# Kernel tuning notes

Measured on AMD Instinct MI355X. Metric: run time of the kernel, lower is better.

## Reference

```python
import jax, jax.numpy as jnp
import numpy as np

N, M, B, C, L, H = 8192, 8192, 16, 512, 64, 8
HEAD_DIM = C // H
PER_BATCH_KEYS = M // B
MASK_VAL = -1000.0  # matches torch masked_fill_ value


def setup_inputs() -> dict:
    key0 = jax.random.key(0)
    ks = jax.random.split(key0, 8)
    query = jax.random.normal(ks[0], (N, C), jnp.float32)
    key = jax.random.normal(ks[1], (M, C), jnp.float32)
    value = jax.random.normal(ks[2], (M, C), jnp.float32)
    # xavier-ish init for projections
    in_proj_weight = jax.random.normal(ks[3], (3 * C, C), jnp.float32) * (1.0 / np.sqrt(C))
    in_proj_bias = jnp.zeros((3 * C,), jnp.float32)
    out_w = jax.random.normal(ks[4], (C, C), jnp.float32) * (1.0 / np.sqrt(C))
    out_b = jnp.zeros((C,), jnp.float32)
    index_pair = jax.random.randint(ks[5], (N, L), 0, PER_BATCH_KEYS).astype(jnp.int32)
    pad = jax.random.uniform(ks[6], (N, L)) < 0.05
    index_pair = jnp.where(pad, jnp.int32(-1), index_pair)
    query_batch_cnt = jnp.full((B,), N // B, jnp.int32)
    key_batch_cnt = jnp.full((B,), PER_BATCH_KEYS, jnp.int32)
    index_pair_batch = jnp.repeat(jnp.arange(B, dtype=jnp.int32), N // B)
    return {
        "query": query, "key": key, "value": value,
        "in_proj_weight": in_proj_weight, "in_proj_bias": in_proj_bias,
        "out_w": out_w, "out_b": out_b,
        "index_pair": index_pair, "query_batch_cnt": query_batch_cnt,
        "key_batch_cnt": key_batch_cnt, "index_pair_batch": index_pair_batch,
    }


def reference(query, key, value, in_proj_weight, in_proj_bias, out_w, out_b,
              index_pair, query_batch_cnt, key_batch_cnt, index_pair_batch):
    embed_dim = query.shape[-1]
    scaling = float(HEAD_DIM) ** -0.5
    # qkv projections (in_proj_weight is [3C, C], applied as F.linear => x @ W.T + b)
    q = (query @ in_proj_weight[:embed_dim].T + in_proj_bias[:embed_dim]) * scaling
    k = key @ in_proj_weight[embed_dim:2 * embed_dim].T + in_proj_bias[embed_dim:2 * embed_dim]
    v = value @ in_proj_weight[2 * embed_dim:].T + in_proj_bias[2 * embed_dim:]
    q = q.reshape(N, H, HEAD_DIM)
    k = k.reshape(M, H, HEAD_DIM)
    v = v.reshape(M, H, HEAD_DIM)
    # local -> global key indices: offset by start of each query's batch key block
    key_start = jnp.cumsum(key_batch_cnt) - key_batch_cnt          # (B,)
    offset = key_start[index_pair_batch]                            # (N,)
    valid = index_pair >= 0                                         # (N, L)
    gidx = jnp.where(valid, index_pair + offset[:, None], 0)        # (N, L), safe gather
    # gather-based scores: (N, L, H)
    scores = jnp.einsum("nhd,nlhd->nlh", q, k[gidx])
    scores = jnp.where(valid[..., None], scores, MASK_VAL)
    w = jax.nn.softmax(scores, axis=1)                              # softmax over neighbors L
    # weighted value sum; masked weights underflow to exactly 0 in fp32
    attn = jnp.einsum("nlh,nlhd->nhd", w, v[gidx]).reshape(N, embed_dim)
    attn = attn @ out_w.T + out_b
    return attn, w.sum(axis=-1) / H
```

## Files before the change

### kernel.cpp

```cpp
#include <hip/hip_runtime.h>
#include <hip/hip_bf16.h>
#include <math.h>

#define NQ 8192
#define MK 8192
#define CD 512
#define LN 64
#define HH 8
#define HD 64
#define BB 16

typedef short short8 __attribute__((ext_vector_type(8)));
typedef float floatx4 __attribute__((ext_vector_type(4)));

__device__ __forceinline__ unsigned short f2bf(float x) {
    unsigned int u = __builtin_bit_cast(unsigned int, x);
    return (unsigned short)((u + 0x7FFFu + ((u >> 16) & 1u)) >> 16);
}
__device__ __forceinline__ unsigned int pkbf(float lo, float hi) {
    float2 f; f.x = lo; f.y = hi;
    __hip_bfloat162 h2 = __float22bfloat162_rn(f);
    unsigned int u;
    __builtin_memcpy(&u, &h2, 4);
    return u;
}
__device__ __forceinline__ float bflo(unsigned int u) {
    return __builtin_bit_cast(float, u << 16);
}
__device__ __forceinline__ float bfhij(unsigned int u) {
    return __builtin_bit_cast(float, u);
}
__device__ __forceinline__ short8 u4s8(uint4 u) {
    short8 s; __builtin_memcpy(&s, &u, 16); return s;
}

__device__ __forceinline__ void gl_lds16(const unsigned short* g, unsigned short* l) {
    __builtin_amdgcn_global_load_lds(
        (const __attribute__((address_space(1))) unsigned int*)g,
        (__attribute__((address_space(3))) unsigned int*)l, 16, 0, 0);
}

struct ConvSeg { const float* src; unsigned short* dst; int n4; };
struct ConvArgs { ConvSeg s[5]; };

__global__ __launch_bounds__(256) void convert_bf16(ConvArgs a) {
    const int seg = blockIdx.y;
    const int i = blockIdx.x * 256 + threadIdx.x;
    if (i >= a.s[seg].n4) return;
    const float4 v = ((const float4*)a.s[seg].src)[i];
    uint2 o; o.x = pkbf(v.x, v.y); o.y = pkbf(v.z, v.w);
    ((uint2*)a.s[seg].dst)[i] = o;
}

__device__ __forceinline__ void gemm_bf_body(const unsigned short* __restrict__ A,
                                             const unsigned short* __restrict__ W,
                                             const float* __restrict__ bias,
                                             float* __restrict__ outf,
                                             unsigned short* __restrict__ outb,
                                             float scale) {
    __shared__ unsigned short As[128 * 64];
    __shared__ unsigned short Bs[128 * 64];

    const int tid  = threadIdx.x;
    const int row0 = blockIdx.x * 128;
    const int col0 = blockIdx.y * 128;

    const int w    = tid >> 6;
    const int lane = tid & 63;
    const int wr   = w >> 1;
    const int wc   = w & 1;
    const int q    = lane >> 4;
    const int ml   = lane & 15;

    const int sr = lane >> 3;
    const int sg = (lane & 7) ^ sr;
    const unsigned short* Ap = A + (size_t)(row0 + w * 32 + sr) * CD + sg * 8;
    const unsigned short* Wp = W + (size_t)(col0 + w * 32 + sr) * CD + sg * 8;
    unsigned short* Asw = &As[(w * 32) * 64];
    unsigned short* Bsw = &Bs[(w * 32) * 64];

    floatx4 acc[4][4];
#pragma unroll
    for (int i = 0; i < 4; ++i)
#pragma unroll
        for (int j = 0; j < 4; ++j)
            acc[i][j] = (floatx4){0.f, 0.f, 0.f, 0.f};

    for (int k0 = 0; k0 < CD; k0 += 64) {
        __syncthreads();
#pragma unroll
        for (int i = 0; i < 4; ++i) {
            gl_lds16(Ap + (size_t)(i * 8) * CD + k0, Asw + i * 8 * 64);
            gl_lds16(Wp + (size_t)(i * 8) * CD + k0, Bsw + i * 8 * 64);
        }
        __syncthreads();

#pragma unroll
        for (int kw = 0; kw < 2; ++kw) {
            short8 af[4], bf[4];
            const int gp = ((kw * 4 + q) ^ (ml & 7)) * 8;
#pragma unroll
            for (int mi = 0; mi < 4; ++mi)
                af[mi] = *(const short8*)&As[(wr * 64 + mi * 16 + ml) * 64 + gp];
#pragma unroll
            for (int ni = 0; ni < 4; ++ni)
                bf[ni] = *(const short8*)&Bs[(wc * 64 + ni * 16 + ml) * 64 + gp];
#pragma unroll
            for (int mi = 0; mi < 4; ++mi)
#pragma unroll
                for (int ni = 0; ni < 4; ++ni)
                    acc[mi][ni] = __builtin_amdgcn_mfma_f32_16x16x32_bf16(
                        af[mi], bf[ni], acc[mi][ni], 0, 0, 0);
        }
    }

    float bv[4];
#pragma unroll
    for (int ni = 0; ni < 4; ++ni)
        bv[ni] = bias[col0 + wc * 64 + ni * 16 + ml];
#pragma unroll
    for (int mi = 0; mi < 4; ++mi) {
#pragma unroll
        for (int ni = 0; ni < 4; ++ni) {
            const int cg = col0 + wc * 64 + ni * 16 + ml;
#pragma unroll
            for (int r = 0; r < 4; ++r) {
                const int rg = row0 + wr * 64 + mi * 16 + q * 4 + r;
                const float val = (acc[mi][ni][r] + bv[ni]) * scale;
                if (outb) outb[(size_t)rg * CD + cg] = f2bf(val);
                else      outf[(size_t)rg * CD + cg] = val;
            }
        }
    }
}

__global__ __launch_bounds__(256) void qkv_gemm(const unsigned short* __restrict__ A_bf,
                                                const unsigned short* __restrict__ w_bf,
                                                const float* __restrict__ bias,
                                                unsigned short* __restrict__ q_bf,
                                                unsigned short* __restrict__ k_bf,
                                                unsigned short* __restrict__ v_bf) {
    const int z = blockIdx.z;
    const unsigned short* A = A_bf + (size_t)z * NQ * CD;
    unsigned short* outb = (z == 0) ? q_bf : ((z == 1) ? k_bf : v_bf);
    gemm_bf_body(A, w_bf + (size_t)z * CD * CD, bias + (size_t)z * CD,
                 nullptr, outb, (z == 0) ? 0.125f : 1.0f);
}

__global__ __launch_bounds__(256) void out_gemm(const unsigned short* __restrict__ A,
                                                const unsigned short* __restrict__ W,
                                                const float* __restrict__ bias,
                                                float* __restrict__ out) {
    gemm_bf_body(A, W, bias, out, nullptr, 1.0f);
}

__global__ __launch_bounds__(512, 4) void attn_kernel(
    const unsigned short* __restrict__ q_bf,
    const unsigned short* __restrict__ k_bf,
    const unsigned short* __restrict__ v_bf,
    const int* __restrict__ index_pair,
    const int* __restrict__ key_batch_cnt,
    const int* __restrict__ index_pair_batch,
    unsigned short* __restrict__ attn_bf,
    float* __restrict__ out2) {
    const int j = blockIdx.x;
    const int n = (j & 7) * (NQ / 8) + (j >> 3);

    const int tid  = threadIdx.x;
    const int h    = tid >> 6;
    const int lane = tid & 63;
    const int quad = lane >> 4;
    const int ml   = lane & 15;

    __shared__ float wmat[HH][LN];
    __shared__ int   gs[LN];
    __shared__ unsigned long long smask;

    if (tid < LN) {
        int incl = (lane < BB) ? key_batch_cnt[lane] : 0;
#pragma unroll
        for (int d = 1; d < BB; d <<= 1) {
            const int t = __shfl_up(incl, d, 64);
            if (lane >= d) incl += t;
        }
        const int batch = index_pair_batch[n];
        int off0 = 0;
        if (batch > 0) off0 = __shfl(incl, batch - 1, 64);
        const int gi = index_pair[n * LN + lane];
        const unsigned long long vm = __ballot(gi >= 0);
        if (lane == 0) smask = vm;
        gs[lane] = (gi >= 0) ? (gi + off0) : 0;
    }
    __syncthreads();

    const char* qp = (const char*)q_bf + (size_t)n * (CD * 2) + h * (HD * 2) + quad * 16;
    const short8 bq0 = u4s8(*(const uint4*)qp);
    const short8 bq1 = u4s8(*(const uint4*)(qp + 64));

    int gr[4];
#pragma unroll
    for (int g = 0; g < 4; ++g) gr[g] = gs[g * 16 + ml];
    uint4 a0[4], a1[4];
#pragma unroll
    for (int g = 0; g < 4; ++g) {
        const char* kp = (const char*)k_bf + (size_t)gr[g] * (CD * 2) + h * (HD * 2) + quad * 16;
        a0[g] = *(const uint4*)kp;
        a1[g] = *(const uint4*)(kp + 64);
    }
    const int r  = lane >> 3;
    const int dg = lane & 7;
    uint4 vv[8];
#pragma unroll
    for (int it = 0; it < 8; ++it) {
        const unsigned int off = (unsigned int)gs[it * 8 + r] * (CD * 2)
                                 + h * (HD * 2) + dg * 16;
        vv[it] = *(const uint4*)((const char*)v_bf + off);
    }

#pragma unroll
    for (int g = 0; g < 4; ++g) {
        floatx4 sa = (floatx4){0.f, 0.f, 0.f, 0.f};
        sa = __builtin_amdgcn_mfma_f32_16x16x32_bf16(u4s8(a0[g]), bq0, sa, 0, 0, 0);
        sa = __builtin_amdgcn_mfma_f32_16x16x32_bf16(u4s8(a1[g]), bq1, sa, 0, 0, 0);
        if (ml == 0) {
#pragma unroll
            for (int rr = 0; rr < 4; ++rr) wmat[h][g * 16 + quad * 4 + rr] = sa[rr];
        }
    }

    float score = wmat[h][lane];
    if (!((smask >> lane) & 1ull)) score = -1000.0f;
    float mx = score;
#pragma unroll
    for (int o = 32; o > 0; o >>= 1) mx = fmaxf(mx, __shfl_xor(mx, o, 64));
    float e = __expf(score - mx);
    float s = e;
#pragma unroll
    for (int o = 32; o > 0; o >>= 1) s += __shfl_xor(s, o, 64);
    const float w = e / s;
    wmat[h][lane] = w;

    float a8[8] = {0.f, 0.f, 0.f, 0.f, 0.f, 0.f, 0.f, 0.f};
#pragma unroll
    for (int it = 0; it < 8; ++it) {
        const float wl = __shfl(w, it * 8 + r, 64);
        a8[0] = fmaf(wl, bflo(vv[it].x),  a8[0]);
        a8[1] = fmaf(wl, bfhij(vv[it].x), a8[1]);
        a8[2] = fmaf(wl, bflo(vv[it].y),  a8[2]);
        a8[3] = fmaf(wl, bfhij(vv[it].y), a8[3]);
        a8[4] = fmaf(wl, bflo(vv[it].z),  a8[4]);
        a8[5] = fmaf(wl, bfhij(vv[it].z), a8[5]);
        a8[6] = fmaf(wl, bflo(vv[it].w),  a8[6]);
        a8[7] = fmaf(wl, bfhij(vv[it].w), a8[7]);
    }
#pragma unroll
    for (int o = 8; o <= 32; o <<= 1)
#pragma unroll
        for (int d = 0; d < 8; ++d) a8[d] += __shfl_xor(a8[d], o, 64);
    attn_bf[(size_t)n * CD + h * HD + dg * 8 + r] = f2bf(a8[r]);

    __syncthreads();
    if (tid < LN) {
        float s8 = 0.f;
#pragma unroll
        for (int hh = 0; hh < HH; ++hh) s8 += wmat[hh][tid];
        out2[(size_t)n * LN + tid] = s8 * (1.0f / HH);
    }
}

extern "C" void kernel_launch(void* const* d_in, const int* in_sizes, int n_in,
                              void* d_out, int out_size, void* d_ws, size_t ws_size,
                              hipStream_t stream) {
    const float* query   = (const float*)d_in[0];
    const float* key     = (const float*)d_in[1];
    const float* value   = (const float*)d_in[2];
    const float* ipw     = (const float*)d_in[3];
    const float* ipb     = (const float*)d_in[4];
    const float* out_w   = (const float*)d_in[5];
    const float* out_b   = (const float*)d_in[6];
    const int*   index_pair       = (const int*)d_in[7];
    const int*   key_batch_cnt    = (const int*)d_in[9];
    const int*   index_pair_batch = (const int*)d_in[10];

    float* out = (float*)d_out;
    unsigned short* q_bf  = (unsigned short*)d_ws;
    unsigned short* k_bf  = q_bf + (size_t)NQ * CD;
    unsigned short* v_bf  = k_bf + (size_t)NQ * CD;
    unsigned short* A_bf  = v_bf + (size_t)NQ * CD;
    unsigned short* w_bf  = A_bf + (size_t)3 * NQ * CD;
    unsigned short* ow_bf = w_bf + (size_t)3 * CD * CD;
    unsigned short* attn_bf = A_bf;

    ConvArgs ca;
    ca.s[0] = {query, A_bf,                       NQ * CD / 4};
    ca.s[1] = {key,   A_bf + (size_t)NQ * CD,     NQ * CD / 4};
    ca.s[2] = {value, A_bf + (size_t)2 * NQ * CD, NQ * CD / 4};
    ca.s[3] = {ipw,   w_bf,                       3 * CD * CD / 4};
    ca.s[4] = {out_w, ow_bf,                      CD * CD / 4};
    dim3 g0(NQ * CD / 4 / 256, 5);
    convert_bf16<<<g0, 256, 0, stream>>>(ca);

    dim3 g1(NQ / 128, CD / 128, 3);
    qkv_gemm<<<g1, 256, 0, stream>>>(A_bf, w_bf, ipb, q_bf, k_bf, v_bf);

    attn_kernel<<<NQ, 512, 0, stream>>>(q_bf, k_bf, v_bf, index_pair,
                                        key_batch_cnt, index_pair_batch,
                                        attn_bf, out + (size_t)NQ * CD);

    dim3 g3(NQ / 128, CD / 128, 1);
    out_gemm<<<g3, 256, 0, stream>>>(attn_bf, ow_bf, out_b, out);
}
```

Baseline: 223.7 us.

## Assign one query per wave looping over heads; shrink GEMM tiles to 64x128

The attention kernel now processes one query per wavefront and loops over all 8 heads, so index loading, batch offset computation and the head-averaged weight sum stay in registers with no block-wide barriers. Previously one head ran per wave in a 512-thread block per query. Both GEMMs switch from 128x128 to 64x128 output tiles, doubling the block count to improve occupancy and load balance. The trade-off is less memory-level parallelism per wave in attention, since heads run sequentially, and lower data reuse per GEMM tile.

```diff
diff --git a/kernel.cpp b/kernel.cpp
--- a/kernel.cpp
+++ b/kernel.cpp
@@ -58,75 +58,74 @@
                                              float* __restrict__ outf,
                                              unsigned short* __restrict__ outb,
                                              float scale) {
-    __shared__ unsigned short As[128 * 64];
+    __shared__ unsigned short As[64 * 64];
     __shared__ unsigned short Bs[128 * 64];
 
     const int tid  = threadIdx.x;
-    const int row0 = blockIdx.x * 128;
+    const int row0 = blockIdx.x * 64;
     const int col0 = blockIdx.y * 128;
 
     const int w    = tid >> 6;
     const int lane = tid & 63;
-    const int wr   = w >> 1;
-    const int wc   = w & 1;
     const int q    = lane >> 4;
     const int ml   = lane & 15;
 
     const int sr = lane >> 3;
     const int sg = (lane & 7) ^ sr;
-    const unsigned short* Ap = A + (size_t)(row0 + w * 32 + sr) * CD + sg * 8;
+    const unsigned short* Ap = A + (size_t)(row0 + w * 16 + sr) * CD + sg * 8;
     const unsigned short* Wp = W + (size_t)(col0 + w * 32 + sr) * CD + sg * 8;
-    unsigned short* Asw = &As[(w * 32) * 64];
+    unsigned short* Asw = &As[(w * 16) * 64];
     unsigned short* Bsw = &Bs[(w * 32) * 64];
 
-    floatx4 acc[4][4];
+    floatx4 acc[4][2];
 #pragma unroll
     for (int i = 0; i < 4; ++i)
 #pragma unroll
-        for (int j = 0; j < 4; ++j)
+        for (int j = 0; j < 2; ++j)
             acc[i][j] = (floatx4){0.f, 0.f, 0.f, 0.f};
 
     for (int k0 = 0; k0 < CD; k0 += 64) {
         __syncthreads();
 #pragma unroll
-        for (int i = 0; i < 4; ++i) {
+        for (int i = 0; i < 2; ++i)
             gl_lds16(Ap + (size_t)(i * 8) * CD + k0, Asw + i * 8 * 64);
+#pragma unroll
+        for (int i = 0; i < 4; ++i)
             gl_lds16(Wp + (size_t)(i * 8) * CD + k0, Bsw + i * 8 * 64);
-        }
         __syncthreads();
 
 #pragma unroll
         for (int kw = 0; kw < 2; ++kw) {
-            short8 af[4], bf[4];
+            short8 af[4], bf[2];
             const int gp = ((kw * 4 + q) ^ (ml & 7)) * 8;
 #pragma unroll
             for (int mi = 0; mi < 4; ++mi)
-                af[mi] = *(const short8*)&As[(wr * 64 + mi * 16 + ml) * 64 + gp];
-#pragma unroll
-            for (int ni = 0; ni < 4; ++ni)
-                bf[ni] = *(const short8*)&Bs[(wc * 64 + ni * 16 + ml) * 64 + gp];
+                af[mi] = *(const short8*)&As[(mi * 16 + ml) * 64 + gp];
+#pragma unroll
+            for (int ni = 0; ni < 2; ++ni)
+                bf[ni] = *(const short8*)&Bs[(w * 32 + ni * 16 + ml) * 64 + gp];
 #pragma unroll
             for (int mi = 0; mi < 4; ++mi)
 #pragma unroll
-                for (int ni = 0; ni < 4; ++ni)
+                for (int ni = 0; ni < 2; ++ni)
                     acc[mi][ni] = __builtin_amdgcn_mfma_f32_16x16x32_bf16(
                         af[mi], bf[ni], acc[mi][ni], 0, 0, 0);
         }
     }
 
-    float bv[4];
-#pragma unroll
-    for (int ni = 0; ni < 4; ++ni)
-        bv[ni] = bias[col0 + wc * 64 + ni * 16 + ml];
+    float bv[2];
+#pragma unroll
+    for (int ni = 0; ni < 2; ++ni)
+        bv[ni] = bias[col0 + w * 32 + ni * 16 + ml];
 #pragma unroll
     for (int mi = 0; mi < 4; ++mi) {
 #pragma unroll
-        for (int ni = 0; ni < 4; ++ni) {
-            const int cg = col0 + wc * 64 + ni * 16 + ml;
-#pragma unroll
-            for (int r = 0; r < 4; ++r) {
-                const int rg = row0 + wr * 64 + mi * 16 + q * 4 + r;
-                const float val = (acc[mi][ni][r] + bv[ni]) * scale;
+        for (int ni = 0; ni < 2; ++ni) {
+            const int cg = col0 + w * 32 + ni * 16 + ml;
+#pragma unroll
+            for (int rr = 0; rr < 4; ++rr) {
+                const int rg = row0 + mi * 16 + q * 4 + rr;
+                const float val = (acc[mi][ni][rr] + bv[ni]) * scale;
                 if (outb) outb[(size_t)rg * CD + cg] = f2bf(val);
                 else      outf[(size_t)rg * CD + cg] = val;
             }
@@ -154,7 +153,7 @@
     gemm_bf_body(A, W, bias, out, nullptr, 1.0f);
 }
 
-__global__ __launch_bounds__(512, 4) void attn_kernel(
+__global__ __launch_bounds__(256) void attn_kernel(
     const unsigned short* __restrict__ q_bf,
     const unsigned short* __restrict__ k_bf,
     const unsigned short* __restrict__ v_bf,
@@ -163,109 +162,107 @@
     const int* __restrict__ index_pair_batch,
     unsigned short* __restrict__ attn_bf,
     float* __restrict__ out2) {
-    const int j = blockIdx.x;
-    const int n = (j & 7) * (NQ / 8) + (j >> 3);
-
     const int tid  = threadIdx.x;
-    const int h    = tid >> 6;
+    const int wid  = tid >> 6;
     const int lane = tid & 63;
+    const int bx   = blockIdx.x;
+    const int n    = (bx & 7) * (NQ / 8) + (bx >> 3) * 4 + wid;
+
     const int quad = lane >> 4;
     const int ml   = lane & 15;
-
-    __shared__ float wmat[HH][LN];
-    __shared__ int   gs[LN];
-    __shared__ unsigned long long smask;
-
-    if (tid < LN) {
-        int incl = (lane < BB) ? key_batch_cnt[lane] : 0;
-#pragma unroll
-        for (int d = 1; d < BB; d <<= 1) {
-            const int t = __shfl_up(incl, d, 64);
-            if (lane >= d) incl += t;
-        }
-        const int batch = index_pair_batch[n];
-        int off0 = 0;
-        if (batch > 0) off0 = __shfl(incl, batch - 1, 64);
-        const int gi = index_pair[n * LN + lane];
-        const unsigned long long vm = __ballot(gi >= 0);
-        if (lane == 0) smask = vm;
-        gs[lane] = (gi >= 0) ? (gi + off0) : 0;
+    const int r    = lane >> 3;
+    const int dg   = lane & 7;
+
+    __shared__ float sc_s[4][LN];
+    float* sc = sc_s[wid];
+
+    int cnt = (lane < BB) ? key_batch_cnt[lane] : 0;
+#pragma unroll
+    for (int d = 1; d < BB; d <<= 1) {
+        const int t = __shfl_up(cnt, d, 64);
+        if (lane >= d) cnt += t;
     }
-    __syncthreads();
-
-    const char* qp = (const char*)q_bf + (size_t)n * (CD * 2) + h * (HD * 2) + quad * 16;
-    const short8 bq0 = u4s8(*(const uint4*)qp);
-    const short8 bq1 = u4s8(*(const uint4*)(qp + 64));
-
-    int gr[4];
-#pragma unroll
-    for (int g = 0; g < 4; ++g) gr[g] = gs[g * 16 + ml];
-    uint4 a0[4], a1[4];
-#pragma unroll
-    for (int g = 0; g < 4; ++g) {
-        const char* kp = (const char*)k_bf + (size_t)gr[g] * (CD * 2) + h * (HD * 2) + quad * 16;
-        a0[g] = *(const uint4*)kp;
-        a1[g] = *(const uint4*)(kp + 64);
+    const int batch = index_pair_batch[n];
+    const int off0  = (batch > 0) ? __shfl(cnt, batch - 1, 64) : 0;
+
+    const int gi = index_pair[n * LN + lane];
+    const unsigned long long vmask = __ballot(gi >= 0);
+    const int g = (gi >= 0) ? (gi + off0) : 0;
+
+    int krow[4];
+#pragma unroll
+    for (int grp = 0; grp < 4; ++grp)
+        krow[grp] = __shfl(g, grp * 16 + ml, 64);
+    int vrow[8];
+#pragma unroll
+    for (int it = 0; it < 8; ++it)
+        vrow[it] = __shfl(g, it * 8 + r, 64);
+
+    const size_t qbase = (size_t)n * CD;
+    float s8 = 0.f;
+
+    for (int h = 0; h < HH; ++h) {
+        const char* qp = (const char*)(q_bf + qbase + h * HD) + quad * 16;
+        const uint4 bq0 = *(const uint4*)qp;
+        const uint4 bq1 = *(const uint4*)(qp + 64);
+        uint4 a0[4], a1[4];
+#pragma unroll
+        for (int grp = 0; grp < 4; ++grp) {
+            const char* kp = (const char*)(k_bf + (size_t)krow[grp] * CD + h * HD) + quad * 16;
+            a0[grp] = *(const uint4*)kp;
+            a1[grp] = *(const uint4*)(kp + 64);
+        }
+        uint4 vv[8];
+#pragma unroll
+        for (int it = 0; it < 8; ++it) {
+            const char* vp = (const char*)(v_bf + (size_t)vrow[it] * CD + h * HD) + dg * 16;
+            vv[it] = *(const uint4*)vp;
+        }
+
+#pragma unroll
+        for (int grp = 0; grp < 4; ++grp) {
+            floatx4 sa = (floatx4){0.f, 0.f, 0.f, 0.f};
+            sa = __builtin_amdgcn_mfma_f32_16x16x32_bf16(u4s8(a0[grp]), u4s8(bq0), sa, 0, 0, 0);
+            sa = __builtin_amdgcn_mfma_f32_16x16x32_bf16(u4s8(a1[grp]), u4s8(bq1), sa, 0, 0, 0);
+            if (ml == 0) {
+#pragma unroll
+                for (int rr = 0; rr < 4; ++rr) sc[grp * 16 + quad * 4 + rr] = sa[rr];
+            }
+        }
+
+        float score = sc[lane];
+        if (!((vmask >> lane) & 1ull)) score = -1000.0f;
+        float mx = score;
+#pragma unroll
+        for (int o = 32; o > 0; o >>= 1) mx = fmaxf(mx, __shfl_xor(mx, o, 64));
+        float e = __expf(score - mx);
+        float s = e;
+#pragma unroll
+        for (int o = 32; o > 0; o >>= 1) s += __shfl_xor(s, o, 64);
+        const float w = e / s;
+        s8 += w;
+
+        float a8[8] = {0.f, 0.f, 0.f, 0.f, 0.f, 0.f, 0.f, 0.f};
+#pragma unroll
+        for (int it = 0; it < 8; ++it) {
+            const float wl = __shfl(w, it * 8 + r, 64);
+            a8[0] = fmaf(wl, bflo(vv[it].x),  a8[0]);
+            a8[1] = fmaf(wl, bfhij(vv[it].x), a8[1]);
+            a8[2] = fmaf(wl, bflo(vv[it].y),  a8[2]);
+            a8[3] = fmaf(wl, bfhij(vv[it].y), a8[3]);
+            a8[4] = fmaf(wl, bflo(vv[it].z),  a8[4]);
+            a8[5] = fmaf(wl, bfhij(vv[it].z), a8[5]);
+            a8[6] = fmaf(wl, bflo(vv[it].w),  a8[6]);
+            a8[7] = fmaf(wl, bfhij(vv[it].w), a8[7]);
+        }
+#pragma unroll
+        for (int o = 8; o <= 32; o <<= 1)
+#pragma unroll
+            for (int d = 0; d < 8; ++d) a8[d] += __shfl_xor(a8[d], o, 64);
+        attn_bf[qbase + h * HD + dg * 8 + r] = f2bf(a8[r]);
     }
-    const int r  = lane >> 3;
-    const int dg = lane & 7;
-    uint4 vv[8];
-#pragma unroll
-    for (int it = 0; it < 8; ++it) {
-        const unsigned int off = (unsigned int)gs[it * 8 + r] * (CD * 2)
-                                 + h * (HD * 2) + dg * 16;
-        vv[it] = *(const uint4*)((const char*)v_bf + off);
-    }
-
-#pragma unroll
-    for (int g = 0; g < 4; ++g) {
-        floatx4 sa = (floatx4){0.f, 0.f, 0.f, 0.f};
-        sa = __builtin_amdgcn_mfma_f32_16x16x32_bf16(u4s8(a0[g]), bq0, sa, 0, 0, 0);
-        sa = __builtin_amdgcn_mfma_f32_16x16x32_bf16(u4s8(a1[g]), bq1, sa, 0, 0, 0);
-        if (ml == 0) {
-#pragma unroll
-            for (int rr = 0; rr < 4; ++rr) wmat[h][g * 16 + quad * 4 + rr] = sa[rr];
-        }
-    }
-
-    float score = wmat[h][lane];
-    if (!((smask >> lane) & 1ull)) score = -1000.0f;
-    float mx = score;
-#pragma unroll
-    for (int o = 32; o > 0; o >>= 1) mx = fmaxf(mx, __shfl_xor(mx, o, 64));
-    float e = __expf(score - mx);
-    float s = e;
-#pragma unroll
-    for (int o = 32; o > 0; o >>= 1) s += __shfl_xor(s, o, 64);
-    const float w = e / s;
-    wmat[h][lane] = w;
-
-    float a8[8] = {0.f, 0.f, 0.f, 0.f, 0.f, 0.f, 0.f, 0.f};
-#pragma unroll
-    for (int it = 0; it < 8; ++it) {
-        const float wl = __shfl(w, it * 8 + r, 64);
-        a8[0] = fmaf(wl, bflo(vv[it].x),  a8[0]);
-        a8[1] = fmaf(wl, bfhij(vv[it].x), a8[1]);
-        a8[2] = fmaf(wl, bflo(vv[it].y),  a8[2]);
-        a8[3] = fmaf(wl, bfhij(vv[it].y), a8[3]);
-        a8[4] = fmaf(wl, bflo(vv[it].z),  a8[4]);
-        a8[5] = fmaf(wl, bfhij(vv[it].z), a8[5]);
-        a8[6] = fmaf(wl, bflo(vv[it].w),  a8[6]);
-        a8[7] = fmaf(wl, bfhij(vv[it].w), a8[7]);
-    }
-#pragma unroll
-    for (int o = 8; o <= 32; o <<= 1)
-#pragma unroll
-        for (int d = 0; d < 8; ++d) a8[d] += __shfl_xor(a8[d], o, 64);
-    attn_bf[(size_t)n * CD + h * HD + dg * 8 + r] = f2bf(a8[r]);
-
-    __syncthreads();
-    if (tid < LN) {
-        float s8 = 0.f;
-#pragma unroll
-        for (int hh = 0; hh < HH; ++hh) s8 += wmat[hh][tid];
-        out2[(size_t)n * LN + tid] = s8 * (1.0f / HH);
-    }
+
+    out2[(size_t)n * LN + lane] = s8 * (1.0f / HH);
 }
 
 extern "C" void kernel_launch(void* const* d_in, const int* in_sizes, int n_in,
@@ -300,13 +297,13 @@
     dim3 g0(NQ * CD / 4 / 256, 5);
     convert_bf16<<<g0, 256, 0, stream>>>(ca);
 
-    dim3 g1(NQ / 128, CD / 128, 3);
+    dim3 g1(NQ / 64, CD / 128, 3);
     qkv_gemm<<<g1, 256, 0, stream>>>(A_bf, w_bf, ipb, q_bf, k_bf, v_bf);
 
-    attn_kernel<<<NQ, 512, 0, stream>>>(q_bf, k_bf, v_bf, index_pair,
-                                        key_batch_cnt, index_pair_batch,
-                                        attn_bf, out + (size_t)NQ * CD);
-
-    dim3 g3(NQ / 128, CD / 128, 1);
+    attn_kernel<<<NQ / 4, 256, 0, stream>>>(q_bf, k_bf, v_bf, index_pair,
+                                            key_batch_cnt, index_pair_batch,
+                                            attn_bf, out + (size_t)NQ * CD);
+
+    dim3 g3(NQ / 64, CD / 128, 1);
     out_gemm<<<g3, 256, 0, stream>>>(attn_bf, ow_bf, out_b, out);
 }
```

Result: no change. 220.9 us (-1.3%).
